# Kernel optimization log

Measured on AMD Instinct MI355X. Metric: run time of the kernel, lower is better.

The kernel has to match this reference:

```python
import math
import jax, jax.numpy as jnp
import numpy as np

B, T, N = 64, 100, 20
NR = N * (N - 1)
D_STATE, D_SHAPE, D_REL = 8, 4, 3
THRESH = 0.35


def _pair_indices(n):
    # (i, j) pairs with i != j, ordered so that relation index
    # r = i*(n-1) + j - (j > i) equals the flattened position.
    ii, jj = np.meshgrid(np.arange(n), np.arange(n), indexing='ij')
    m = ii != jj
    return ii[m], jj[m]  # each [n*(n-1)]


def setup_inputs() -> dict:
    key = jax.random.key(0)
    k1, k2, k3 = jax.random.split(key, 3)
    objects_state = jax.random.uniform(k1, (B, T, N, D_STATE), dtype=jnp.float32)
    objects_shape = jax.random.normal(k2, (B, T, N, D_SHAPE), dtype=jnp.float32)
    relation_info = jax.random.normal(k3, (B, T, NR, D_REL), dtype=jnp.float32)
    return {"objects_state": objects_state, "objects_shape": objects_shape,
            "relation_info": relation_info}


def reference(objects_state, objects_shape, relation_info):
    dt = objects_state.dtype
    i_idx, j_idx = _pair_indices(N)

    # cdist over xy positions, then threshold (diagonal is exactly 0 -> excluded by nonzero)
    pos = objects_state[..., 0:2]                                   # [B,T,N,2]
    d = jnp.linalg.norm(pos[..., :, None, :] - pos[..., None, :, :], axis=-1)  # [B,T,N,N]
    adj = (d < THRESH) & (d > 0)
    mask = adj[..., i_idx, j_idx].astype(dt)                        # [B,T,NR]

    eye = jnp.eye(N, dtype=dt)
    receiver_relations = mask[..., None] * eye[i_idx]               # [B,T,NR,N]
    sender_relations = mask[..., None] * eye[j_idx]                 # [B,T,NR,N]

    # identity scaler
    data_state, data_shape = objects_state, objects_shape

    senders_state = jnp.einsum('btrn,btnd->btrd', sender_relations, data_state)
    receivers_state = jnp.einsum('btrn,btnd->btrd', receiver_relations, data_state)
    senders_shape = jnp.einsum('btrn,btnd->btrd', sender_relations, data_shape)
    receivers_shape = jnp.einsum('btrn,btnd->btrd', receiver_relations, data_shape)

    recv_ang = receivers_state[..., 2:3]                            # [B,T,NR,1]
    half_pi = jnp.asarray(math.pi / 2, dtype=dt)
    b1 = jnp.concatenate([jnp.cos(recv_ang), jnp.sin(recv_ang)], axis=-1)
    b2 = jnp.concatenate([jnp.cos(recv_ang + half_pi), jnp.sin(recv_ang + half_pi)], axis=-1)
    basis = jnp.stack([b1, b2], axis=-2)                            # [B,T,NR,2,2]

    diff_state = senders_state - receivers_state
    diff_pos = diff_state[..., 0:2]
    diff_vel = diff_state[..., 3:5]
    control = senders_state[..., 6:8]
    angle_diff = diff_state[..., 2:3]
    angle_diff_vel = diff_state[..., 5:6]

    temp = jnp.stack([diff_pos, diff_vel, control], axis=-1)        # [B,T,NR,2,3]
    tfed = jnp.einsum('btrij,btrjk->btrik', basis, temp)            # [B,T,NR,2,3]
    diff_pos, diff_vel, control = tfed[..., 0], tfed[..., 1], tfed[..., 2]

    diff_angle_2d = jnp.concatenate([jnp.sin(2 * angle_diff), jnp.cos(2 * angle_diff)], axis=-1)
    diff_state = jnp.concatenate([diff_pos, diff_vel, control, diff_angle_2d, angle_diff_vel], axis=-1)
    rel_data = jnp.concatenate([relation_info, diff_state, receivers_shape, senders_shape], axis=-1)

    obj_ang = data_state[..., 2:3]                                  # [B,T,N,1]
    ob1 = jnp.concatenate([jnp.cos(obj_ang), jnp.sin(obj_ang)], axis=-1)
    ob2 = jnp.concatenate([jnp.cos(obj_ang + half_pi), jnp.sin(obj_ang + half_pi)], axis=-1)
    object_basis = jnp.stack([ob1, ob2], axis=-2)                   # [B,T,N,2,2]
    obj_vel = data_state[..., 3:5]
    obj_vel_tfed = jnp.einsum('btnij,btnj->btni', object_basis, obj_vel)
    obj_data = jnp.concatenate([obj_vel_tfed, data_state[..., 5:6], data_shape], axis=-1)

    return rel_data, obj_data, receiver_relations, sender_relations
```

## Files before the change

kernel.cpp:

```cpp
#include <hip/hip_runtime.h>
#include <math.h>

#define BB 64
#define TT 100
#define NN 20
#define NRR 380
#define NBT (BB * TT)

typedef float f32x4 __attribute__((ext_vector_type(4)));

__global__ __launch_bounds__(256) void fused_kernel(
    const float* __restrict__ state,
    const float* __restrict__ shape,
    const float* __restrict__ relinfo,
    float* __restrict__ out)
{
    const int blk  = blockIdx.x;
    const int role = blk / NBT;
    const int bt   = blk - role * NBT;
    const int tid  = threadIdx.x;

    const float THRESH  = 0.35f;
    const float HALF_PI = 1.57079632679489661923f;

    const size_t REL_SZ = (size_t)NBT * NRR * 20;
    const size_t OBJ_SZ = (size_t)NBT * NN * 7;

    __shared__ float  s_state[NN * 8];
    __shared__ float  s_shape[NN * 4];
    __shared__ float4 s_row4[NRR * 5];
    __shared__ float  s_mask[NRR];
    __shared__ int    s_col[NRR];

    if (role == 0) {
        const int   r2v = tid + 256;
        const int   r2c = (r2v < NRR) ? r2v : (NRR - 1);
        const float* rbase = relinfo + (size_t)bt * NRR * 3;
        const float ra0 = rbase[tid * 3 + 0];
        const float ra1 = rbase[tid * 3 + 1];
        const float ra2 = rbase[tid * 3 + 2];
        const float rb0 = rbase[r2c * 3 + 0];
        const float rb1 = rbase[r2c * 3 + 1];
        const float rb2 = rbase[r2c * 3 + 2];

        if (tid < NN * 8)               s_state[tid]          = state[(size_t)bt * NN * 8 + tid];
        else if (tid < NN * 8 + NN * 4) s_shape[tid - NN * 8] = shape[(size_t)bt * NN * 4 + (tid - NN * 8)];
        __syncthreads();

        f32x4* relb = (f32x4*)out + (size_t)bt * (NRR * 5);
        float* objb = out + REL_SZ + (size_t)bt * (NN * 7);

        if (tid < NN * 7) {
            const int n = tid / 7;
            const int c = tid - n * 7;
            float v;
            if (c < 2) {
                const float ang = s_state[n * 8 + 2];
                const float a   = (c == 0) ? ang : (ang + HALF_PI);
                v = cosf(a) * s_state[n * 8 + 3] + sinf(a) * s_state[n * 8 + 4];
            } else if (c == 2) {
                v = s_state[n * 8 + 5];
            } else {
                v = s_shape[n * 4 + (c - 3)];
            }
            objb[tid] = v;
        }

        for (int pass = 0; pass < 2; ++pass) {
            const int r = (pass == 0) ? tid : r2v;
            if (r < NRR) {
                const float f0 = (pass == 0) ? ra0 : rb0;
                const float f1 = (pass == 0) ? ra1 : rb1;
                const float f2 = (pass == 0) ? ra2 : rb2;

                const int i = r / 19;
                const int l = r - i * 19;
                const int j = (l < i) ? l : (l + 1);

                const float* si = &s_state[i * 8];
                const float* sj = &s_state[j * 8];

                const float dx = si[0] - sj[0];
                const float dy = si[1] - sj[1];
                const float d  = sqrtf(dx * dx + dy * dy);
                const float mask = (d < THRESH && d > 0.0f) ? 1.0f : 0.0f;

                const float dpx   = mask * (sj[0] - si[0]);
                const float dpy   = mask * (sj[1] - si[1]);
                const float adiff = mask * (sj[2] - si[2]);
                const float dvx   = mask * (sj[3] - si[3]);
                const float dvy   = mask * (sj[4] - si[4]);
                const float adv   = mask * (sj[5] - si[5]);
                const float cx    = mask * sj[6];
                const float cy    = mask * sj[7];

                const float rang = mask * si[2];
                const float c1 = cosf(rang),           s1 = sinf(rang);
                const float c2 = cosf(rang + HALF_PI), s2 = sinf(rang + HALF_PI);

                float4 w0, w1, w2, w3, w4;
                w0.x = f0; w0.y = f1; w0.z = f2;
                w0.w = c1 * dpx + s1 * dpy;
                w1.x = c2 * dpx + s2 * dpy;
                w1.y = c1 * dvx + s1 * dvy;
                w1.z = c2 * dvx + s2 * dvy;
                w1.w = c1 * cx  + s1 * cy;
                w2.x = c2 * cx  + s2 * cy;
                w2.y = sinf(2.0f * adiff);
                w2.z = cosf(2.0f * adiff);
                w2.w = adv;
                w3.x = mask * s_shape[i * 4 + 0];
                w3.y = mask * s_shape[i * 4 + 1];
                w3.z = mask * s_shape[i * 4 + 2];
                w3.w = mask * s_shape[i * 4 + 3];
                w4.x = mask * s_shape[j * 4 + 0];
                w4.y = mask * s_shape[j * 4 + 1];
                w4.z = mask * s_shape[j * 4 + 2];
                w4.w = mask * s_shape[j * 4 + 3];

                float4* row = &s_row4[r * 5];
                row[0] = w0; row[1] = w1; row[2] = w2; row[3] = w3; row[4] = w4;
            }
        }
        __syncthreads();

#pragma unroll
        for (int k = 0; k < 8; ++k) {
            const int idx = tid + k * 256;
            if (idx < NRR * 5) {
                const float4 w = s_row4[idx];
                f32x4 wv;
                wv.x = w.x; wv.y = w.y; wv.z = w.z; wv.w = w.w;
                relb[idx] = wv;
            }
        }
    } else {
        if (tid < NN * 2) {
            const int n = tid >> 1, c = tid & 1;
            s_state[tid] = state[(size_t)bt * NN * 8 + n * 8 + c];
        }
        __syncthreads();

        for (int r = tid; r < NRR; r += 256) {
            const int i = r / 19;
            const int l = r - i * 19;
            const int j = (l < i) ? l : (l + 1);
            const float dx = s_state[i * 2 + 0] - s_state[j * 2 + 0];
            const float dy = s_state[i * 2 + 1] - s_state[j * 2 + 1];
            const float d  = sqrtf(dx * dx + dy * dy);
            s_mask[r] = (d < THRESH && d > 0.0f) ? 1.0f : 0.0f;
            s_col[r]  = (role == 1) ? i : j;
        }
        __syncthreads();

        f32x4* dst = (f32x4*)(out + REL_SZ + OBJ_SZ + (size_t)(role - 1) * REL_SZ)
                     + (size_t)bt * (NRR * 5);

#pragma unroll
        for (int k = 0; k < 8; ++k) {
            const int idx = tid + k * 256;
            if (idx < NRR * 5) {
                const int r  = idx / 5;
                const int qb = (idx - r * 5) * 4;
                const float m = s_mask[r];
                const int   c = s_col[r];
                f32x4 v;
                v.x = (c == qb + 0) ? m : 0.0f;
                v.y = (c == qb + 1) ? m : 0.0f;
                v.z = (c == qb + 2) ? m : 0.0f;
                v.w = (c == qb + 3) ? m : 0.0f;
                dst[idx] = v;
            }
        }
    }
}

extern "C" void kernel_launch(void* const* d_in, const int* in_sizes, int n_in,
                              void* d_out, int out_size, void* d_ws, size_t ws_size,
                              hipStream_t stream) {
    const float* state = (const float*)d_in[0];
    const float* shp   = (const float*)d_in[1];
    const float* rel   = (const float*)d_in[2];
    float* out = (float*)d_out;
    fused_kernel<<<dim3(NBT * 3), dim3(256), 0, stream>>>(state, shp, rel, out);
}
```

Baseline: 118.8 us.

## Use grid-stride flat loop for relation one-hot output blocks

Replaces the per-(b,t) blocks that write the receiver and sender one-hot matrices with a fixed pool of 4096 blocks per matrix. Each thread runs a grid-stride loop over the flattened float4 output index and recomputes the distance mask directly from global state for every element, with no shared memory and no barriers. This removes the per-block sync overhead and idle threads in the pure-store blocks and shrinks the grid. The cost is redundant mask computation and extra integer divisions per element.

```diff
diff --git a/kernel.cpp b/kernel.cpp
--- a/kernel.cpp
+++ b/kernel.cpp
@@ -6,6 +6,8 @@
 #define NN 20
 #define NRR 380
 #define NBT (BB * TT)
+#define QT  (NBT * NRR * 5)
+#define OHB 4096
 
 typedef float f32x4 __attribute__((ext_vector_type(4)));
 
@@ -15,10 +17,8 @@
     const float* __restrict__ relinfo,
     float* __restrict__ out)
 {
-    const int blk  = blockIdx.x;
-    const int role = blk / NBT;
-    const int bt   = blk - role * NBT;
-    const int tid  = threadIdx.x;
+    const int blk = blockIdx.x;
+    const int tid = threadIdx.x;
 
     const float THRESH  = 0.35f;
     const float HALF_PI = 1.57079632679489661923f;
@@ -29,10 +29,10 @@
     __shared__ float  s_state[NN * 8];
     __shared__ float  s_shape[NN * 4];
     __shared__ float4 s_row4[NRR * 5];
-    __shared__ float  s_mask[NRR];
-    __shared__ int    s_col[NRR];
 
-    if (role == 0) {
+    if (blk < NBT) {
+        const int bt = blk;
+
         const int   r2v = tid + 256;
         const int   r2c = (r2v < NRR) ? r2v : (NRR - 1);
         const float* rbase = relinfo + (size_t)bt * NRR * 3;
@@ -135,42 +135,36 @@
             }
         }
     } else {
-        if (tid < NN * 2) {
-            const int n = tid >> 1, c = tid & 1;
-            s_state[tid] = state[(size_t)bt * NN * 8 + n * 8 + c];
-        }
-        __syncthreads();
+        const int  rb   = blk - NBT;
+        const bool recv = (rb < OHB);
+        const int  base = recv ? rb : (rb - OHB);
 
-        for (int r = tid; r < NRR; r += 256) {
-            const int i = r / 19;
-            const int l = r - i * 19;
-            const int j = (l < i) ? l : (l + 1);
-            const float dx = s_state[i * 2 + 0] - s_state[j * 2 + 0];
-            const float dy = s_state[i * 2 + 1] - s_state[j * 2 + 1];
+        f32x4* dst = (f32x4*)(out + REL_SZ + OBJ_SZ + (recv ? 0 : REL_SZ));
+
+        for (int idx = base * 256 + tid; idx < QT; idx += OHB * 256) {
+            const int bt  = idx / 1900;
+            const int rem = idx - bt * 1900;
+            const int r   = rem / 5;
+            const int q   = rem - r * 5;
+            const int i   = r / 19;
+            const int l   = r - i * 19;
+            const int j   = (l < i) ? l : (l + 1);
+
+            const float2 pi = *(const float2*)(state + (size_t)bt * (NN * 8) + i * 8);
+            const float2 pj = *(const float2*)(state + (size_t)bt * (NN * 8) + j * 8);
+            const float dx = pi.x - pj.x;
+            const float dy = pi.y - pj.y;
             const float d  = sqrtf(dx * dx + dy * dy);
-            s_mask[r] = (d < THRESH && d > 0.0f) ? 1.0f : 0.0f;
-            s_col[r]  = (role == 1) ? i : j;
-        }
-        __syncthreads();
+            const float m  = (d < THRESH && d > 0.0f) ? 1.0f : 0.0f;
 
-        f32x4* dst = (f32x4*)(out + REL_SZ + OBJ_SZ + (size_t)(role - 1) * REL_SZ)
-                     + (size_t)bt * (NRR * 5);
-
-#pragma unroll
-        for (int k = 0; k < 8; ++k) {
-            const int idx = tid + k * 256;
-            if (idx < NRR * 5) {
-                const int r  = idx / 5;
-                const int qb = (idx - r * 5) * 4;
-                const float m = s_mask[r];
-                const int   c = s_col[r];
-                f32x4 v;
-                v.x = (c == qb + 0) ? m : 0.0f;
-                v.y = (c == qb + 1) ? m : 0.0f;
-                v.z = (c == qb + 2) ? m : 0.0f;
-                v.w = (c == qb + 3) ? m : 0.0f;
-                dst[idx] = v;
-            }
+            const int c  = recv ? i : j;
+            const int qb = q * 4;
+            f32x4 v;
+            v.x = (c == qb + 0) ? m : 0.0f;
+            v.y = (c == qb + 1) ? m : 0.0f;
+            v.z = (c == qb + 2) ? m : 0.0f;
+            v.w = (c == qb + 3) ? m : 0.0f;
+            dst[idx] = v;
         }
     }
 }
@@ -182,5 +176,5 @@
     const float* shp   = (const float*)d_in[1];
     const float* rel   = (const float*)d_in[2];
     float* out = (float*)d_out;
-    fused_kernel<<<dim3(NBT * 3), dim3(256), 0, stream>>>(state, shp, rel, out);
+    fused_kernel<<<dim3(NBT + 2 * OHB), dim3(256), 0, stream>>>(state, shp, rel, out);
 }
```

Measured after the change: 120.2 us. Within noise of the previous version (+1.2%).
